# Performance work log

Measured on AMD Instinct MI355X. Metric: run time of the kernel, lower is better.

The kernel has to match this reference:

```python
import jax, jax.numpy as jnp
from jax import lax
import numpy as np

B, C, H, W = 32, 64, 80, 80


def setup_inputs() -> dict:
    key = jax.random.key(0)
    ks = jax.random.split(key, 9)
    x = jax.random.normal(ks[0], (B, C, H, W), dtype=jnp.float32)
    # gammas are zero-init Parameters in torch; use small random values so the
    # recurrence is non-trivial but numerically stable (spectral radius ~0.4).
    g = lambda k: jax.random.normal(k, (C, C), dtype=jnp.float32) * 0.05
    return {"x": x,
            "g1": g(ks[1]), "g2": g(ks[2]),
            "g4": g(ks[3]), "g5": g(ks[4]),
            "g7": g(ks[5]), "g8": g(ks[6]),
            "g10": g(ks[7]), "g11": g(ks[8])}


def _scan_dir(xh, gv, gh, apply_relu):
    """Row-major DAG recurrence over xh: [H, W, C, B].
    h[i,j] = act(x[i,j] + gv @ h[i-1,j] + gh @ h[i,j-1]).
    Zero carry at boundaries exactly reproduces the i>0 / j>0 guards
    (gamma @ 0 == 0)."""
    def row_step(prev_row, x_row):
        # prev_row: [W, C, B] -- vertical contribution for the whole row at once
        up = jnp.einsum('cd,wdb->wcb', gv, prev_row)
        def col_step(left, inp):
            xc, upc = inp                      # [C, B] each
            h = xc + upc + gh @ left
            if apply_relu:
                h = jax.nn.relu(h)
            return h, h
        _, row = lax.scan(col_step, jnp.zeros_like(x_row[0]), (x_row, up))
        return row, row
    _, out = lax.scan(row_step, jnp.zeros_like(xh[0]), xh)
    return out


def reference(x, g1, g2, g4, g5, g7, g8, g10, g11):
    # torch permutes to [C, B, H, W]; we use [H, W, C, B] so scans run over
    # leading axes and each cell is the same [C, B] matrix as hse[:, :, i, j].
    xh = jnp.transpose(x, (2, 3, 1, 0))  # [H, W, C, B]
    # SE: i forward, j forward, ReLU
    hse = _scan_dir(xh, g1, g2, True)
    # NE: i reversed, j forward, ReLU -> flip H
    hne = _scan_dir(xh[::-1], g4, g5, True)[::-1]
    # NW: i reversed, j reversed, ReLU -> flip H and W
    hnw = _scan_dir(xh[::-1, ::-1], g7, g8, True)[::-1, ::-1]
    # SW: i forward, j reversed, NO ReLU (omitted in the original code) -> flip W
    hsw = _scan_dir(xh[:, ::-1], g10, g11, False)[:, ::-1]
    out = hse + hne + hnw + hsw
    return jnp.transpose(out, (3, 2, 0, 1))  # back to [B, C, H, W]
```

## Files before the change

kernel.cpp:

```cpp
#include <hip/hip_runtime.h>
#include <stdint.h>

#define HH 80
#define WW 80
#define CC 64
#define BB 32
#define NDIAG (HH + WW - 1)
#define SLICE (HH * WW * CC)
#define NCW 5
#define NTHREADS 512

typedef _Float16 f16;
typedef _Float16 f16x8 __attribute__((ext_vector_type(8)));
typedef _Float16 f16x4 __attribute__((ext_vector_type(4)));
typedef float floatx4 __attribute__((ext_vector_type(4)));

struct GPtrs { const float* p[8]; };

__global__ __launch_bounds__(256) void xpose_kernel(const float* __restrict__ x,
                                                    f16* __restrict__ xT) {
  const int bi = blockIdx.x;
  const int b = bi / HH, i = bi - b * HH;
  __shared__ float tile[WW][CC + 1];
  const float* xp = x + ((size_t)(b * CC) * HH + i) * WW;
  for (int idx = threadIdx.x; idx < CC * WW; idx += 256) {
    const int c = idx / WW, j = idx - c * WW;
    tile[j][c] = xp[(size_t)c * (HH * WW) + j];
  }
  __syncthreads();
  f16* op = xT + (size_t)(b * HH + i) * WW * CC;
  for (int idx = threadIdx.x; idx < (WW * CC) / 4; idx += 256) {
    const int j = idx >> 4, m = idx & 15;
    f16x4 v;
    v[0] = (f16)tile[j][m * 4 + 0];
    v[1] = (f16)tile[j][m * 4 + 1];
    v[2] = (f16)tile[j][m * 4 + 2];
    v[3] = (f16)tile[j][m * 4 + 3];
    *(f16x4*)(op + j * CC + m * 4) = v;
  }
}

__global__ __launch_bounds__(NTHREADS, 1) void dag_kernel(const f16* __restrict__ xT,
                                                          GPtrs g,
                                                          f16* __restrict__ scratch) {
  const int blk = blockIdx.x;
  const int dir = blk >> 5;
  const int b   = blk & 31;
  const int tid = threadIdx.x;
  const int wv   = tid >> 6;
  const int lane = tid & 63;
  const int l15  = lane & 15;
  const int quad = lane >> 4;

  const bool fi      = (dir == 1) || (dir == 2);
  const bool fj      = (dir == 2) || (dir == 3);
  const bool do_relu = (dir != 3);
  const float* __restrict__ gv = g.p[2 * dir];
  const float* __restrict__ gh = g.p[2 * dir + 1];

  __align__(16) __shared__ f16 hbuf[2][HH + 2][CC + 8];
  __align__(16) __shared__ f16 xring[2][HH][CC + 8];

  for (int idx = tid; idx < 2 * (HH + 2) * (CC + 8); idx += NTHREADS)
    (&hbuf[0][0][0])[idx] = (f16)0.0f;

  const f16* const xTb = xT + (size_t)b * SLICE;
  f16* const sbase = scratch + (size_t)blk * SLICE;

  auto cellOff = [&](int dd, int cell) -> int {
    const int lo = max(0, dd - (WW - 1));
    const int hi = min(dd, HH - 1);
    const int ipc = min(max(cell, lo), hi);
    const int jp = dd - ipc;
    const int io1 = fi ? (HH - 1 - ipc) : ipc;
    const int jo1 = fj ? (WW - 1 - jp) : jp;
    return io1 * WW + jo1;
  };

  f16x8 Av[4][2], Ah[4][2];
  f16x8 xb[4];
  int ucell[4];
  const int cq = quad * 4;
  const int cm = lane >> 3;
  const int c8 = (lane & 7) * 8;

  if (wv < NCW) {
#pragma unroll
    for (int cb = 0; cb < 4; ++cb) {
      const int row = cb * 16 + l15;
      const float* pv = gv + row * CC;
      const float* ph = gh + row * CC;
#pragma unroll
      for (int jj = 0; jj < 8; ++jj) {
        Av[cb][0][jj] = (f16)pv[quad * 8 + jj];
        Av[cb][1][jj] = (f16)pv[32 + quad * 8 + jj];
        Ah[cb][0][jj] = (f16)ph[quad * 8 + jj];
        Ah[cb][1][jj] = (f16)ph[32 + quad * 8 + jj];
      }
    }
  } else {
    const int wio = wv - NCW;
#pragma unroll
    for (int k = 0; k < 4; ++k) ucell[k] = min(wio + 3 * k, 9) * 8 + cm;
    f16x8 b0[4];
#pragma unroll
    for (int k = 0; k < 4; ++k)
      b0[k] = *(const f16x8*)(xTb + (cellOff(0, ucell[k]) << 6) + c8);
#pragma unroll
    for (int k = 0; k < 4; ++k)
      *(f16x8*)&xring[0][ucell[k]][c8] = b0[k];
#pragma unroll
    for (int k = 0; k < 4; ++k)
      xb[k] = *(const f16x8*)(xTb + (cellOff(1, ucell[k]) << 6) + c8);
  }

  __syncthreads();

  for (int d = 0; d < NDIAG; ++d) {
    const int p = d & 1, q = p ^ 1;
    const int ilo = max(0, d - (WW - 1));
    const int ihi = min(d, HH - 1);

    if (wv < NCW) {
      const int ntiles = ((ihi - ilo) >> 4) + 1;
      if (wv < ntiles) {
        const int ip  = ilo + wv * 16 + l15;
        const int ipx = min(ip, ihi);
        const int su  = min(ip, HH + 1);
        const int sl  = min(ip + 1, HH + 1);
        const f16x8 bu0 = *(const f16x8*)&hbuf[q][su][quad * 8];
        const f16x8 bu1 = *(const f16x8*)&hbuf[q][su][32 + quad * 8];
        const f16x8 bl0 = *(const f16x8*)&hbuf[q][sl][quad * 8];
        const f16x8 bl1 = *(const f16x8*)&hbuf[q][sl][32 + quad * 8];
        const bool ok = (ip <= ihi);
#pragma unroll
        for (int cb = 0; cb < 4; ++cb) {
          const f16x4 xv = *(const f16x4*)&xring[p][ipx][cb * 16 + cq];
          floatx4 a;
          a[0] = (float)xv[0]; a[1] = (float)xv[1];
          a[2] = (float)xv[2]; a[3] = (float)xv[3];
          a = __builtin_amdgcn_mfma_f32_16x16x32_f16(Av[cb][0], bu0, a, 0, 0, 0);
          a = __builtin_amdgcn_mfma_f32_16x16x32_f16(Av[cb][1], bu1, a, 0, 0, 0);
          a = __builtin_amdgcn_mfma_f32_16x16x32_f16(Ah[cb][0], bl0, a, 0, 0, 0);
          a = __builtin_amdgcn_mfma_f32_16x16x32_f16(Ah[cb][1], bl1, a, 0, 0, 0);
          float h0 = a[0], h1 = a[1], h2 = a[2], h3 = a[3];
          if (do_relu) {
            h0 = fmaxf(h0, 0.f); h1 = fmaxf(h1, 0.f);
            h2 = fmaxf(h2, 0.f); h3 = fmaxf(h3, 0.f);
          }
          f16x4 hw;
          hw[0] = (f16)h0; hw[1] = (f16)h1; hw[2] = (f16)h2; hw[3] = (f16)h3;
          if (ok) *(f16x4*)&hbuf[p][ip + 1][cb * 16 + cq] = hw;
        }
      }
    } else {
      f16x8 nb[4];
      const int dpre = min(d + 2, NDIAG - 1);
#pragma unroll
      for (int k = 0; k < 4; ++k)
        nb[k] = *(const f16x8*)(xTb + (cellOff(dpre, ucell[k]) << 6) + c8);
      const int s1 = (d + 1) & 1;
#pragma unroll
      for (int k = 0; k < 4; ++k)
        *(f16x8*)&xring[s1][ucell[k]][c8] = xb[k];
      if (d >= 1) {
        const int dF = d - 1;
        const int lo = max(0, dF - (WW - 1)), hi = min(dF, HH - 1);
#pragma unroll
        for (int k = 0; k < 4; ++k) {
          const int ipc = min(max(ucell[k], lo), hi);
          const f16x8 hv = *(const f16x8*)&hbuf[q][ipc + 1][c8];
          *(f16x8*)(sbase + (cellOff(dF, ucell[k]) << 6) + c8) = hv;
        }
      }
#pragma unroll
      for (int k = 0; k < 4; ++k) xb[k] = nb[k];
    }

    __builtin_amdgcn_s_waitcnt(0xC07F);
    __builtin_amdgcn_s_barrier();
  }

  if (wv >= NCW) {
    const int dF = NDIAG - 1;
    const int lo = max(0, dF - (WW - 1)), hi = min(dF, HH - 1);
#pragma unroll
    for (int k = 0; k < 4; ++k) {
      const int ipc = min(max(ucell[k], lo), hi);
      const f16x8 hv = *(const f16x8*)&hbuf[dF & 1][ipc + 1][c8];
      *(f16x8*)(sbase + (cellOff(dF, ucell[k]) << 6) + c8) = hv;
    }
  }
}

__global__ __launch_bounds__(256) void reduce_kernel(const f16* __restrict__ s,
                                                     float* __restrict__ out) {
  const int bi = blockIdx.x;
  const int b = bi / HH, i = bi - b * HH;
  __shared__ float tile[WW][CC + 1];
  const size_t dstride = (size_t)BB * SLICE;
  const f16* p = s + (size_t)b * SLICE + (size_t)i * (WW * CC);
  for (int idx = threadIdx.x; idx < (WW * CC) / 8; idx += 256) {
    const int j = idx >> 3, c8 = (idx & 7) * 8;
    const size_t off = (size_t)j * CC + c8;
    const f16x8 a0 = *(const f16x8*)(p + off);
    const f16x8 a1 = *(const f16x8*)(p + off + dstride);
    const f16x8 a2 = *(const f16x8*)(p + off + 2 * dstride);
    const f16x8 a3 = *(const f16x8*)(p + off + 3 * dstride);
#pragma unroll
    for (int k = 0; k < 8; ++k)
      tile[j][c8 + k] = (float)a0[k] + (float)a1[k] + (float)a2[k] + (float)a3[k];
  }
  __syncthreads();
  float* op = out + ((size_t)(b * CC) * HH + i) * WW;
  const int c  = threadIdx.x >> 2;
  const int jb = (threadIdx.x & 3) * 4;
#pragma unroll
  for (int k = 0; k < 5; ++k) {
    const int j0 = jb + k * 16;
    floatx4 v;
    v[0] = tile[j0 + 0][c];
    v[1] = tile[j0 + 1][c];
    v[2] = tile[j0 + 2][c];
    v[3] = tile[j0 + 3][c];
    *(floatx4*)(op + (size_t)c * (HH * WW) + j0) = v;
  }
}

extern "C" void kernel_launch(void* const* d_in, const int* in_sizes, int n_in,
                              void* d_out, int out_size, void* d_ws, size_t ws_size,
                              hipStream_t stream) {
  const float* x = (const float*)d_in[0];
  GPtrs g;
  for (int k = 0; k < 8; ++k) g.p[k] = (const float*)d_in[k + 1];
  f16* xT = (f16*)d_ws;
  f16* scratch = xT + (size_t)BB * SLICE;

  xpose_kernel<<<BB * HH, 256, 0, stream>>>(x, xT);
  dag_kernel<<<4 * BB, NTHREADS, 0, stream>>>((const f16*)xT, g, scratch);
  reduce_kernel<<<BB * HH, 256, 0, stream>>>((const f16*)scratch, (float*)d_out);
}
```

Measured before the change: 252.4 us.

## Fuse input transpose into DAG kernel and drop dedicated I/O waves

Removes the separate transpose kernel. Compute waves now prefetch fp32 input directly from the NCHW tensor into registers two diagonals ahead, and write their outputs straight to global scratch instead of handing them to separate I/O waves through an LDS ring. The block shrinks to five compute waves, and the four MFMAs are split into two independent accumulator chains to shorten the dependency path. The cost is strided, uncoalesced global loads (one channel stride per element) and stores issued from the critical-path waves.

```diff
diff --git a/kernel.cpp b/kernel.cpp
--- a/kernel.cpp
+++ b/kernel.cpp
@@ -8,7 +8,7 @@
 #define NDIAG (HH + WW - 1)
 #define SLICE (HH * WW * CC)
 #define NCW 5
-#define NTHREADS 512
+#define NTHREADS 320
 
 typedef _Float16 f16;
 typedef _Float16 f16x8 __attribute__((ext_vector_type(8)));
@@ -17,30 +17,7 @@
 
 struct GPtrs { const float* p[8]; };
 
-__global__ __launch_bounds__(256) void xpose_kernel(const float* __restrict__ x,
-                                                    f16* __restrict__ xT) {
-  const int bi = blockIdx.x;
-  const int b = bi / HH, i = bi - b * HH;
-  __shared__ float tile[WW][CC + 1];
-  const float* xp = x + ((size_t)(b * CC) * HH + i) * WW;
-  for (int idx = threadIdx.x; idx < CC * WW; idx += 256) {
-    const int c = idx / WW, j = idx - c * WW;
-    tile[j][c] = xp[(size_t)c * (HH * WW) + j];
-  }
-  __syncthreads();
-  f16* op = xT + (size_t)(b * HH + i) * WW * CC;
-  for (int idx = threadIdx.x; idx < (WW * CC) / 4; idx += 256) {
-    const int j = idx >> 4, m = idx & 15;
-    f16x4 v;
-    v[0] = (f16)tile[j][m * 4 + 0];
-    v[1] = (f16)tile[j][m * 4 + 1];
-    v[2] = (f16)tile[j][m * 4 + 2];
-    v[3] = (f16)tile[j][m * 4 + 3];
-    *(f16x4*)(op + j * CC + m * 4) = v;
-  }
-}
-
-__global__ __launch_bounds__(NTHREADS, 1) void dag_kernel(const f16* __restrict__ xT,
+__global__ __launch_bounds__(NTHREADS, 1) void dag_kernel(const float* __restrict__ x,
                                                           GPtrs g,
                                                           f16* __restrict__ scratch) {
   const int blk = blockIdx.x;
@@ -51,6 +28,7 @@
   const int lane = tid & 63;
   const int l15  = lane & 15;
   const int quad = lane >> 4;
+  const int cq   = quad * 4;
 
   const bool fi      = (dir == 1) || (dir == 2);
   const bool fj      = (dir == 2) || (dir == 3);
@@ -59,138 +37,102 @@
   const float* __restrict__ gh = g.p[2 * dir + 1];
 
   __align__(16) __shared__ f16 hbuf[2][HH + 2][CC + 8];
-  __align__(16) __shared__ f16 xring[2][HH][CC + 8];
 
-  for (int idx = tid; idx < 2 * (HH + 2) * (CC + 8); idx += NTHREADS)
-    (&hbuf[0][0][0])[idx] = (f16)0.0f;
+  {
+    f16x8 z = {};
+    f16x8* hb = (f16x8*)&hbuf[0][0][0];
+    for (int idx = tid; idx < (2 * (HH + 2) * (CC + 8)) / 8; idx += NTHREADS)
+      hb[idx] = z;
+  }
 
-  const f16* const xTb = xT + (size_t)b * SLICE;
+  const float* const xb_ = x + (size_t)b * (CC * HH * WW);
   f16* const sbase = scratch + (size_t)blk * SLICE;
 
-  auto cellOff = [&](int dd, int cell) -> int {
-    const int lo = max(0, dd - (WW - 1));
-    const int hi = min(dd, HH - 1);
-    const int ipc = min(max(cell, lo), hi);
-    const int jp = dd - ipc;
-    const int io1 = fi ? (HH - 1 - ipc) : ipc;
-    const int jo1 = fj ? (WW - 1 - jp) : jp;
-    return io1 * WW + jo1;
+  f16x8 Av[4][2], Ah[4][2];
+#pragma unroll
+  for (int cb = 0; cb < 4; ++cb) {
+    const int row = cb * 16 + l15;
+    const float* pv = gv + row * CC;
+    const float* ph = gh + row * CC;
+#pragma unroll
+    for (int jj = 0; jj < 8; ++jj) {
+      Av[cb][0][jj] = (f16)pv[quad * 8 + jj];
+      Av[cb][1][jj] = (f16)pv[32 + quad * 8 + jj];
+      Ah[cb][0][jj] = (f16)ph[quad * 8 + jj];
+      Ah[cb][1][jj] = (f16)ph[32 + quad * 8 + jj];
+    }
+  }
+
+  floatx4 XA[4], XB[4];
+  auto prefetch = [&](int dd, floatx4 (&X)[4]) {
+    const int lo2 = max(0, dd - (WW - 1));
+    const int hi2 = min(dd, HH - 1);
+    const int ipc = min(lo2 + wv * 16 + l15, hi2);
+    const int jp2 = dd - ipc;
+    const int io2 = fi ? (HH - 1 - ipc) : ipc;
+    const int jo2 = fj ? (WW - 1 - jp2) : jp2;
+    const float* xp = xb_ + (io2 * WW + jo2);
+#pragma unroll
+    for (int cb = 0; cb < 4; ++cb)
+#pragma unroll
+      for (int r = 0; r < 4; ++r)
+        X[cb][r] = xp[(cb * 16 + cq + r) * (HH * WW)];
   };
 
-  f16x8 Av[4][2], Ah[4][2];
-  f16x8 xb[4];
-  int ucell[4];
-  const int cq = quad * 4;
-  const int cm = lane >> 3;
-  const int c8 = (lane & 7) * 8;
+  prefetch(0, XA);
+  prefetch(1, XB);
+  __syncthreads();
 
-  if (wv < NCW) {
+  auto step = [&](int d, int par, floatx4 (&X)[4]) {
+    const int ilo = max(0, d - (WW - 1));
+    const int ihi = min(d, HH - 1);
+    const int ntiles = ((ihi - ilo) >> 4) + 1;
+    if (wv < ntiles) {
+      const int ip  = ilo + wv * 16 + l15;
+      const int ipa = min(ip, ihi);
+      const int su  = min(ip, HH + 1);
+      const int sl  = min(ip + 1, HH + 1);
+      const f16x8 bu0 = *(const f16x8*)&hbuf[par ^ 1][su][quad * 8];
+      const f16x8 bu1 = *(const f16x8*)&hbuf[par ^ 1][su][32 + quad * 8];
+      const f16x8 bl0 = *(const f16x8*)&hbuf[par ^ 1][sl][quad * 8];
+      const f16x8 bl1 = *(const f16x8*)&hbuf[par ^ 1][sl][32 + quad * 8];
+      const bool ok = (ip <= ihi);
+      const int jp  = d - ipa;
+      const int io1 = fi ? (HH - 1 - ipa) : ipa;
+      const int jo1 = fj ? (WW - 1 - jp) : jp;
+      f16* const so = sbase + ((io1 * WW + jo1) << 6);
 #pragma unroll
-    for (int cb = 0; cb < 4; ++cb) {
-      const int row = cb * 16 + l15;
-      const float* pv = gv + row * CC;
-      const float* ph = gh + row * CC;
-#pragma unroll
-      for (int jj = 0; jj < 8; ++jj) {
-        Av[cb][0][jj] = (f16)pv[quad * 8 + jj];
-        Av[cb][1][jj] = (f16)pv[32 + quad * 8 + jj];
-        Ah[cb][0][jj] = (f16)ph[quad * 8 + jj];
-        Ah[cb][1][jj] = (f16)ph[32 + quad * 8 + jj];
+      for (int cb = 0; cb < 4; ++cb) {
+        floatx4 a1 = X[cb];
+        floatx4 a2 = {0.f, 0.f, 0.f, 0.f};
+        a1 = __builtin_amdgcn_mfma_f32_16x16x32_f16(Av[cb][0], bu0, a1, 0, 0, 0);
+        a2 = __builtin_amdgcn_mfma_f32_16x16x32_f16(Ah[cb][0], bl0, a2, 0, 0, 0);
+        a1 = __builtin_amdgcn_mfma_f32_16x16x32_f16(Av[cb][1], bu1, a1, 0, 0, 0);
+        a2 = __builtin_amdgcn_mfma_f32_16x16x32_f16(Ah[cb][1], bl1, a2, 0, 0, 0);
+        float h0 = a1[0] + a2[0], h1 = a1[1] + a2[1];
+        float h2 = a1[2] + a2[2], h3 = a1[3] + a2[3];
+        if (do_relu) {
+          h0 = fmaxf(h0, 0.f); h1 = fmaxf(h1, 0.f);
+          h2 = fmaxf(h2, 0.f); h3 = fmaxf(h3, 0.f);
+        }
+        f16x4 hw;
+        hw[0] = (f16)h0; hw[1] = (f16)h1; hw[2] = (f16)h2; hw[3] = (f16)h3;
+        if (ok) {
+          *(f16x4*)&hbuf[par][ip + 1][cb * 16 + cq] = hw;
+          *(f16x4*)(so + cb * 16 + cq) = hw;
+        }
       }
     }
-  } else {
-    const int wio = wv - NCW;
-#pragma unroll
-    for (int k = 0; k < 4; ++k) ucell[k] = min(wio + 3 * k, 9) * 8 + cm;
-    f16x8 b0[4];
-#pragma unroll
-    for (int k = 0; k < 4; ++k)
-      b0[k] = *(const f16x8*)(xTb + (cellOff(0, ucell[k]) << 6) + c8);
-#pragma unroll
-    for (int k = 0; k < 4; ++k)
-      *(f16x8*)&xring[0][ucell[k]][c8] = b0[k];
-#pragma unroll
-    for (int k = 0; k < 4; ++k)
-      xb[k] = *(const f16x8*)(xTb + (cellOff(1, ucell[k]) << 6) + c8);
-  }
-
-  __syncthreads();
-
-  for (int d = 0; d < NDIAG; ++d) {
-    const int p = d & 1, q = p ^ 1;
-    const int ilo = max(0, d - (WW - 1));
-    const int ihi = min(d, HH - 1);
-
-    if (wv < NCW) {
-      const int ntiles = ((ihi - ilo) >> 4) + 1;
-      if (wv < ntiles) {
-        const int ip  = ilo + wv * 16 + l15;
-        const int ipx = min(ip, ihi);
-        const int su  = min(ip, HH + 1);
-        const int sl  = min(ip + 1, HH + 1);
-        const f16x8 bu0 = *(const f16x8*)&hbuf[q][su][quad * 8];
-        const f16x8 bu1 = *(const f16x8*)&hbuf[q][su][32 + quad * 8];
-        const f16x8 bl0 = *(const f16x8*)&hbuf[q][sl][quad * 8];
-        const f16x8 bl1 = *(const f16x8*)&hbuf[q][sl][32 + quad * 8];
-        const bool ok = (ip <= ihi);
-#pragma unroll
-        for (int cb = 0; cb < 4; ++cb) {
-          const f16x4 xv = *(const f16x4*)&xring[p][ipx][cb * 16 + cq];
-          floatx4 a;
-          a[0] = (float)xv[0]; a[1] = (float)xv[1];
-          a[2] = (float)xv[2]; a[3] = (float)xv[3];
-          a = __builtin_amdgcn_mfma_f32_16x16x32_f16(Av[cb][0], bu0, a, 0, 0, 0);
-          a = __builtin_amdgcn_mfma_f32_16x16x32_f16(Av[cb][1], bu1, a, 0, 0, 0);
-          a = __builtin_amdgcn_mfma_f32_16x16x32_f16(Ah[cb][0], bl0, a, 0, 0, 0);
-          a = __builtin_amdgcn_mfma_f32_16x16x32_f16(Ah[cb][1], bl1, a, 0, 0, 0);
-          float h0 = a[0], h1 = a[1], h2 = a[2], h3 = a[3];
-          if (do_relu) {
-            h0 = fmaxf(h0, 0.f); h1 = fmaxf(h1, 0.f);
-            h2 = fmaxf(h2, 0.f); h3 = fmaxf(h3, 0.f);
-          }
-          f16x4 hw;
-          hw[0] = (f16)h0; hw[1] = (f16)h1; hw[2] = (f16)h2; hw[3] = (f16)h3;
-          if (ok) *(f16x4*)&hbuf[p][ip + 1][cb * 16 + cq] = hw;
-        }
-      }
-    } else {
-      f16x8 nb[4];
-      const int dpre = min(d + 2, NDIAG - 1);
-#pragma unroll
-      for (int k = 0; k < 4; ++k)
-        nb[k] = *(const f16x8*)(xTb + (cellOff(dpre, ucell[k]) << 6) + c8);
-      const int s1 = (d + 1) & 1;
-#pragma unroll
-      for (int k = 0; k < 4; ++k)
-        *(f16x8*)&xring[s1][ucell[k]][c8] = xb[k];
-      if (d >= 1) {
-        const int dF = d - 1;
-        const int lo = max(0, dF - (WW - 1)), hi = min(dF, HH - 1);
-#pragma unroll
-        for (int k = 0; k < 4; ++k) {
-          const int ipc = min(max(ucell[k], lo), hi);
-          const f16x8 hv = *(const f16x8*)&hbuf[q][ipc + 1][c8];
-          *(f16x8*)(sbase + (cellOff(dF, ucell[k]) << 6) + c8) = hv;
-        }
-      }
-#pragma unroll
-      for (int k = 0; k < 4; ++k) xb[k] = nb[k];
-    }
-
+    prefetch(min(d + 2, NDIAG - 1), X);
     __builtin_amdgcn_s_waitcnt(0xC07F);
     __builtin_amdgcn_s_barrier();
+  };
+
+  for (int d = 0; d < NDIAG - 1; d += 2) {
+    step(d, 0, XA);
+    step(d + 1, 1, XB);
   }
-
-  if (wv >= NCW) {
-    const int dF = NDIAG - 1;
-    const int lo = max(0, dF - (WW - 1)), hi = min(dF, HH - 1);
-#pragma unroll
-    for (int k = 0; k < 4; ++k) {
-      const int ipc = min(max(ucell[k], lo), hi);
-      const f16x8 hv = *(const f16x8*)&hbuf[dF & 1][ipc + 1][c8];
-      *(f16x8*)(sbase + (cellOff(dF, ucell[k]) << 6) + c8) = hv;
-    }
-  }
+  step(NDIAG - 1, 0, XA);
 }
 
 __global__ __launch_bounds__(256) void reduce_kernel(const f16* __restrict__ s,
@@ -233,10 +175,8 @@
   const float* x = (const float*)d_in[0];
   GPtrs g;
   for (int k = 0; k < 8; ++k) g.p[k] = (const float*)d_in[k + 1];
-  f16* xT = (f16*)d_ws;
-  f16* scratch = xT + (size_t)BB * SLICE;
+  f16* scratch = (f16*)d_ws;
 
-  xpose_kernel<<<BB * HH, 256, 0, stream>>>(x, xT);
-  dag_kernel<<<4 * BB, NTHREADS, 0, stream>>>((const f16*)xT, g, scratch);
+  dag_kernel<<<4 * BB, NTHREADS, 0, stream>>>(x, g, scratch);
   reduce_kernel<<<BB * HH, 256, 0, stream>>>((const f16*)scratch, (float*)d_out);
 }
```

Measured after the change: 690.7 us. +173.7%, slower.

## Process three anti-diagonals per barrier with skewed per-wave tiles

Applied to the files above, without the earlier changes.

The DAG wavefront kernel now advances three anti-diagonals per block-wide barrier instead of one. Each compute wave owns a skewed 14-row window, so its cells on successive diagonals depend only on its own earlier outputs, and only a wave-local LDS wait is needed between phases. The I/O waves move three diagonals of x and h per step through six-slot LDS rings. The MFMA chain is split into two independent accumulators and run at raised priority. Barrier count drops about threefold, at the cost of more LDS, overlapping boundary rows computed redundantly, and more complex indexing.

```diff
diff --git a/kernel.cpp b/kernel.cpp
--- a/kernel.cpp
+++ b/kernel.cpp
@@ -7,8 +7,11 @@
 #define BB 32
 #define NDIAG (HH + WW - 1)
 #define SLICE (HH * WW * CC)
-#define NCW 5
-#define NTHREADS 512
+#define NCW 6
+#define NIOW 3
+#define NTHREADS ((NCW + NIOW) * 64)
+#define NIV 53
+#define PAD 72
 
 typedef _Float16 f16;
 typedef _Float16 f16x8 __attribute__((ext_vector_type(8)));
@@ -16,6 +19,9 @@
 typedef float floatx4 __attribute__((ext_vector_type(4)));
 
 struct GPtrs { const float* p[8]; };
+
+#define WAITLGKM() do { __builtin_amdgcn_s_waitcnt(0xC07F); \
+                        __builtin_amdgcn_sched_barrier(0); } while (0)
 
 __global__ __launch_bounds__(256) void xpose_kernel(const float* __restrict__ x,
                                                     f16* __restrict__ xT) {
@@ -51,6 +57,7 @@
   const int lane = tid & 63;
   const int l15  = lane & 15;
   const int quad = lane >> 4;
+  const int cq   = quad * 4;
 
   const bool fi      = (dir == 1) || (dir == 2);
   const bool fj      = (dir == 2) || (dir == 3);
@@ -58,11 +65,15 @@
   const float* __restrict__ gv = g.p[2 * dir];
   const float* __restrict__ gh = g.p[2 * dir + 1];
 
-  __align__(16) __shared__ f16 hbuf[2][HH + 2][CC + 8];
-  __align__(16) __shared__ f16 xring[2][HH][CC + 8];
-
-  for (int idx = tid; idx < 2 * (HH + 2) * (CC + 8); idx += NTHREADS)
-    (&hbuf[0][0][0])[idx] = (f16)0.0f;
+  __align__(16) __shared__ f16 hbuf[6][HH + 2][PAD];
+  __align__(16) __shared__ f16 xring[6][HH][PAD];
+
+  {
+    f16x8 z = {};
+    f16x8* hb = (f16x8*)&hbuf[0][0][0];
+    for (int idx = tid; idx < (6 * (HH + 2) * PAD) / 8; idx += NTHREADS)
+      hb[idx] = z;
+  }
 
   const f16* const xTb = xT + (size_t)b * SLICE;
   f16* const sbase = scratch + (size_t)blk * SLICE;
@@ -78,9 +89,7 @@
   };
 
   f16x8 Av[4][2], Ah[4][2];
-  f16x8 xb[4];
-  int ucell[4];
-  const int cq = quad * 4;
+  f16x8 xb[10];
   const int cm = lane >> 3;
   const int c8 = (lane & 7) * 8;
 
@@ -100,81 +109,110 @@
     }
   } else {
     const int wio = wv - NCW;
-#pragma unroll
-    for (int k = 0; k < 4; ++k) ucell[k] = min(wio + 3 * k, 9) * 8 + cm;
-    f16x8 b0[4];
-#pragma unroll
-    for (int k = 0; k < 4; ++k)
-      b0[k] = *(const f16x8*)(xTb + (cellOff(0, ucell[k]) << 6) + c8);
-#pragma unroll
-    for (int k = 0; k < 4; ++k)
-      *(f16x8*)&xring[0][ucell[k]][c8] = b0[k];
-#pragma unroll
-    for (int k = 0; k < 4; ++k)
-      xb[k] = *(const f16x8*)(xTb + (cellOff(1, ucell[k]) << 6) + c8);
+    f16x8 b0[10];
+#pragma unroll
+    for (int k = 0; k < 10; ++k) {
+      const int gk = wio + 3 * k, q = gk / 10, ch = gk - q * 10;
+      b0[k] = *(const f16x8*)(xTb + (cellOff(q, ch * 8 + cm) << 6) + c8);
+    }
+#pragma unroll
+    for (int k = 0; k < 10; ++k) {
+      const int gk = wio + 3 * k, q = gk / 10, ch = gk - q * 10;
+      const int ipw = min(ch * 8 + cm, min(q, HH - 1));
+      *(f16x8*)&xring[q][ipw][c8] = b0[k];
+    }
+#pragma unroll
+    for (int k = 0; k < 10; ++k) {
+      const int gk = wio + 3 * k, q = gk / 10, ch = gk - q * 10;
+      xb[k] = *(const f16x8*)(xTb + (cellOff(3 + q, ch * 8 + cm) << 6) + c8);
+    }
   }
 
   __syncthreads();
 
-  for (int d = 0; d < NDIAG; ++d) {
-    const int p = d & 1, q = p ^ 1;
-    const int ilo = max(0, d - (WW - 1));
-    const int ihi = min(d, HH - 1);
+  auto cphase = [&](int hi, int a, int wlim, int rb, int wb, int xs) {
+    const int ip  = a + l15;
+    const int ipx = min(ip, hi);
+    const int su  = min(ip, HH + 1);
+    const int sl  = min(ip + 1, HH + 1);
+    const f16x8 bu0 = *(const f16x8*)&hbuf[rb][su][quad * 8];
+    const f16x8 bu1 = *(const f16x8*)&hbuf[rb][su][32 + quad * 8];
+    const f16x8 bl0 = *(const f16x8*)&hbuf[rb][sl][quad * 8];
+    const f16x8 bl1 = *(const f16x8*)&hbuf[rb][sl][32 + quad * 8];
+    const bool ok = (l15 < wlim) && (ip <= hi);
+    __builtin_amdgcn_s_setprio(1);
+#pragma unroll
+    for (int cb = 0; cb < 4; ++cb) {
+      const f16x4 xv = *(const f16x4*)&xring[xs][ipx][cb * 16 + cq];
+      floatx4 a1v;
+      a1v[0] = (float)xv[0]; a1v[1] = (float)xv[1];
+      a1v[2] = (float)xv[2]; a1v[3] = (float)xv[3];
+      floatx4 a2v = {0.f, 0.f, 0.f, 0.f};
+      a1v = __builtin_amdgcn_mfma_f32_16x16x32_f16(Av[cb][0], bu0, a1v, 0, 0, 0);
+      a2v = __builtin_amdgcn_mfma_f32_16x16x32_f16(Ah[cb][0], bl0, a2v, 0, 0, 0);
+      a1v = __builtin_amdgcn_mfma_f32_16x16x32_f16(Av[cb][1], bu1, a1v, 0, 0, 0);
+      a2v = __builtin_amdgcn_mfma_f32_16x16x32_f16(Ah[cb][1], bl1, a2v, 0, 0, 0);
+      float h0 = a1v[0] + a2v[0], h1 = a1v[1] + a2v[1];
+      float h2 = a1v[2] + a2v[2], h3 = a1v[3] + a2v[3];
+      if (do_relu) {
+        h0 = fmaxf(h0, 0.f); h1 = fmaxf(h1, 0.f);
+        h2 = fmaxf(h2, 0.f); h3 = fmaxf(h3, 0.f);
+      }
+      f16x4 hw;
+      hw[0] = (f16)h0; hw[1] = (f16)h1; hw[2] = (f16)h2; hw[3] = (f16)h3;
+      if (ok) *(f16x4*)&hbuf[wb][ip + 1][cb * 16 + cq] = hw;
+    }
+    __builtin_amdgcn_s_setprio(0);
+  };
+
+  for (int t = 0; t < NIV; ++t) {
+    const int D  = 3 * t;
+    const int sA = (t & 1) * 3;
+    const int sB = 3 - sA;
 
     if (wv < NCW) {
-      const int ntiles = ((ihi - ilo) >> 4) + 1;
-      if (wv < ntiles) {
-        const int ip  = ilo + wv * 16 + l15;
-        const int ipx = min(ip, ihi);
-        const int su  = min(ip, HH + 1);
-        const int sl  = min(ip + 1, HH + 1);
-        const f16x8 bu0 = *(const f16x8*)&hbuf[q][su][quad * 8];
-        const f16x8 bu1 = *(const f16x8*)&hbuf[q][su][32 + quad * 8];
-        const f16x8 bl0 = *(const f16x8*)&hbuf[q][sl][quad * 8];
-        const f16x8 bl1 = *(const f16x8*)&hbuf[q][sl][32 + quad * 8];
-        const bool ok = (ip <= ihi);
-#pragma unroll
-        for (int cb = 0; cb < 4; ++cb) {
-          const f16x4 xv = *(const f16x4*)&xring[p][ipx][cb * 16 + cq];
-          floatx4 a;
-          a[0] = (float)xv[0]; a[1] = (float)xv[1];
-          a[2] = (float)xv[2]; a[3] = (float)xv[3];
-          a = __builtin_amdgcn_mfma_f32_16x16x32_f16(Av[cb][0], bu0, a, 0, 0, 0);
-          a = __builtin_amdgcn_mfma_f32_16x16x32_f16(Av[cb][1], bu1, a, 0, 0, 0);
-          a = __builtin_amdgcn_mfma_f32_16x16x32_f16(Ah[cb][0], bl0, a, 0, 0, 0);
-          a = __builtin_amdgcn_mfma_f32_16x16x32_f16(Ah[cb][1], bl1, a, 0, 0, 0);
-          float h0 = a[0], h1 = a[1], h2 = a[2], h3 = a[3];
-          if (do_relu) {
-            h0 = fmaxf(h0, 0.f); h1 = fmaxf(h1, 0.f);
-            h2 = fmaxf(h2, 0.f); h3 = fmaxf(h3, 0.f);
-          }
-          f16x4 hw;
-          hw[0] = (f16)h0; hw[1] = (f16)h1; hw[2] = (f16)h2; hw[3] = (f16)h3;
-          if (ok) *(f16x4*)&hbuf[p][ip + 1][cb * 16 + cq] = hw;
+      const int lo0 = max(0, D - (WW - 1)), hi0 = min(D, HH - 1);
+      const int lo1 = max(0, D - (WW - 2)), hi1 = min(D + 1, HH - 1);
+      const int lo2 = max(0, D - (WW - 3)), hi2 = min(D + 2, HH - 1);
+      const int a2 = lo2 + 14 * wv;
+      const int a1 = max(lo1, a2 - 1);
+      const int a0 = max(lo0, a1 - 1);
+      if (a0 <= hi0) cphase(hi0, a0, 16, sB + 2, sA + 0, sA + 0);
+      WAITLGKM();
+      if (a1 <= hi1) cphase(hi1, a1, 15, sA + 0, sA + 1, sA + 1);
+      WAITLGKM();
+      if (a2 <= hi2) cphase(hi2, a2, 14, sA + 1, sA + 2, sA + 2);
+    } else {
+      const int wio = wv - NCW;
+      f16x8 nb[10];
+#pragma unroll
+      for (int k = 0; k < 10; ++k) {
+        const int gk = wio + 3 * k, q = gk / 10, ch = gk - q * 10;
+        const int ld = min(D + 6 + q, NDIAG - 1);
+        nb[k] = *(const f16x8*)(xTb + (cellOff(ld, ch * 8 + cm) << 6) + c8);
+      }
+#pragma unroll
+      for (int k = 0; k < 10; ++k) {
+        const int gk = wio + 3 * k, q = gk / 10, ch = gk - q * 10;
+        const int wd = D + 3 + q;
+        const int lo = max(0, wd - (WW - 1)), hi = min(wd, HH - 1);
+        const int ipw = min(max(ch * 8 + cm, lo), hi);
+        *(f16x8*)&xring[sB + q][ipw][c8] = xb[k];
+      }
+      if (t >= 1) {
+#pragma unroll
+        for (int k = 0; k < 10; ++k) {
+          const int gk = wio + 3 * k, q = gk / 10, ch = gk - q * 10;
+          const int cell = ch * 8 + cm;
+          const int fd = D - 3 + q;
+          const int lo = max(0, fd - (WW - 1)), hi = min(fd, HH - 1);
+          const int ipc = min(max(cell, lo), hi);
+          const f16x8 hv = *(const f16x8*)&hbuf[sB + q][ipc + 1][c8];
+          *(f16x8*)(sbase + (cellOff(fd, cell) << 6) + c8) = hv;
         }
       }
-    } else {
-      f16x8 nb[4];
-      const int dpre = min(d + 2, NDIAG - 1);
-#pragma unroll
-      for (int k = 0; k < 4; ++k)
-        nb[k] = *(const f16x8*)(xTb + (cellOff(dpre, ucell[k]) << 6) + c8);
-      const int s1 = (d + 1) & 1;
-#pragma unroll
-      for (int k = 0; k < 4; ++k)
-        *(f16x8*)&xring[s1][ucell[k]][c8] = xb[k];
-      if (d >= 1) {
-        const int dF = d - 1;
-        const int lo = max(0, dF - (WW - 1)), hi = min(dF, HH - 1);
-#pragma unroll
-        for (int k = 0; k < 4; ++k) {
-          const int ipc = min(max(ucell[k], lo), hi);
-          const f16x8 hv = *(const f16x8*)&hbuf[q][ipc + 1][c8];
-          *(f16x8*)(sbase + (cellOff(dF, ucell[k]) << 6) + c8) = hv;
-        }
-      }
-#pragma unroll
-      for (int k = 0; k < 4; ++k) xb[k] = nb[k];
+#pragma unroll
+      for (int k = 0; k < 10; ++k) xb[k] = nb[k];
     }
 
     __builtin_amdgcn_s_waitcnt(0xC07F);
@@ -182,13 +220,16 @@
   }
 
   if (wv >= NCW) {
-    const int dF = NDIAG - 1;
-    const int lo = max(0, dF - (WW - 1)), hi = min(dF, HH - 1);
-#pragma unroll
-    for (int k = 0; k < 4; ++k) {
-      const int ipc = min(max(ucell[k], lo), hi);
-      const f16x8 hv = *(const f16x8*)&hbuf[dF & 1][ipc + 1][c8];
-      *(f16x8*)(sbase + (cellOff(dF, ucell[k]) << 6) + c8) = hv;
+    const int wio = wv - NCW;
+#pragma unroll
+    for (int k = 0; k < 10; ++k) {
+      const int gk = wio + 3 * k, q = gk / 10, ch = gk - q * 10;
+      const int cell = ch * 8 + cm;
+      const int fd = 156 + q;
+      const int lo = max(0, fd - (WW - 1)), hi = min(fd, HH - 1);
+      const int ipc = min(max(cell, lo), hi);
+      const f16x8 hv = *(const f16x8*)&hbuf[q][ipc + 1][c8];
+      *(f16x8*)(sbase + (cellOff(fd, cell) << 6) + c8) = hv;
     }
   }
 }
```

Result: slower. 533.8 us (+111.5%).
